# Performance work log

Hardware: AMD Instinct MI355X
Metric: run time of the kernel (lower is better)

Reference implementation:

```python
import jax, jax.numpy as jnp
import numpy as np

BOLTZMAN = 0.001987191
NATOM = 200000
L = 64  # filter_length


def setup_inputs() -> dict:
    key = jax.random.key(0)
    k1, k2, k3, k4, k5 = jax.random.split(key, 5)
    v = jax.random.normal(k1, (NATOM, 3), dtype=jnp.float32)
    mass = jnp.ones((NATOM, 3), dtype=jnp.float32)
    h = jax.random.uniform(k2, (1, 1, L), dtype=jnp.float32) * 0.002  # ~gamma_uniform scale
    v_list = jax.random.normal(k3, (NATOM * 3, 1, L), dtype=jnp.float32)
    w_list = jax.random.normal(k4, (NATOM * 3, 1, L), dtype=jnp.float32)
    w_new = jax.random.normal(k5, (NATOM, 3), dtype=jnp.float32)
    return {"v": v, "T": 300, "dt": 1, "mass": mass, "h": h,
            "v_list": v_list, "w_list": w_list, "w_new": w_new}


def reference(v, T, dt, mass, h, v_list, w_list, w_new):
    h1 = h[0, 0]  # [L]
    # construct_memory: conv1d(pad(h,(0,L-1)), h) == autocorrelation lags 0..L-1
    mk = jnp.correlate(h1, h1, mode="full")[L - 1:]  # [L]
    mk = mk * (mass[0, 0] * BOLTZMAN * T)
    # roll ring buffers left by 1 and write newest sample in last slot
    vl = jnp.concatenate([v_list[:, 0, 1:], v.reshape(-1, 1)], axis=1)   # [3N, L]
    wl = jnp.concatenate([w_list[:, 0, 1:], w_new.reshape(-1, 1)], axis=1)  # [3N, L]
    # conv1d(x, k.flip(2)) with len-L kernel -> single dot product per channel:
    # out = sum_t x[t] * k[L-1-t]
    friction = -(vl @ mk[::-1])          # [3N]
    random = wl @ h1[::-1]               # [3N]
    delta_v_langevin = (friction + random).reshape(v.shape)
    return delta_v_langevin
```

## Files before the change

### kernel.cpp

```cpp
#include <hip/hip_runtime.h>

#define BOLTZMAN 0.001987191f

__global__ void gle_setup(const float* __restrict__ h,
                          const float* __restrict__ mass,
                          const int* __restrict__ T,
                          float* __restrict__ coef) {
    __shared__ float sh[64];
    int t = threadIdx.x;
    if (t < 64) sh[t] = h[t];
    __syncthreads();
    if (t < 64) {
        float scale = mass[0] * BOLTZMAN * (float)T[0];
        int lag = (t == 0) ? 0 : (64 - t);
        float s = 0.0f;
        for (int k = 0; k + lag < 64; ++k) s += sh[k] * sh[k + lag];
        coef[t]      = -scale * s;
        coef[64 + t] = (t == 0) ? sh[0] : sh[64 - t];
    }
}

__global__ void __launch_bounds__(256) gle_main(
    const float* __restrict__ v, const float* __restrict__ w_new,
    const float* __restrict__ v_list, const float* __restrict__ w_list,
    const float* __restrict__ coef, float* __restrict__ out, int nrows)
{
    int row = blockIdx.x * 16 + (threadIdx.x >> 4);
    int c = threadIdx.x & 15;
    if (row >= nrows) return;

    const float4* A4 = (const float4*)coef;
    const float4* B4 = (const float4*)(coef + 64);
    float4 a = A4[c];
    float4 b = B4[c];

    float4 x = ((const float4*)(v_list + (size_t)row * 64))[c];
    float4 y = ((const float4*)(w_list + (size_t)row * 64))[c];
    if (c == 0) { x.x = v[row]; y.x = w_new[row]; }

    float s = a.x * x.x + a.y * x.y + a.z * x.z + a.w * x.w
            + b.x * y.x + b.y * y.y + b.z * y.z + b.w * y.w;

    s += __shfl_xor(s, 1);
    s += __shfl_xor(s, 2);
    s += __shfl_xor(s, 4);
    s += __shfl_xor(s, 8);

    if (c == 0) out[row] = s;
}

extern "C" void kernel_launch(void* const* d_in, const int* in_sizes, int n_in,
                              void* d_out, int out_size, void* d_ws, size_t ws_size,
                              hipStream_t stream) {
    const float* v      = (const float*)d_in[0];
    const int*   T      = (const int*)d_in[1];
    const float* mass   = (const float*)d_in[3];
    const float* h      = (const float*)d_in[4];
    const float* v_list = (const float*)d_in[5];
    const float* w_list = (const float*)d_in[6];
    const float* w_new  = (const float*)d_in[7];
    float* out  = (float*)d_out;
    float* coef = (float*)d_ws;

    int nrows = in_sizes[0];

    gle_setup<<<1, 64, 0, stream>>>(h, mass, T, coef);

    int blocks = (nrows + 15) / 16;
    gle_main<<<blocks, 256, 0, stream>>>(v, w_new, v_list, w_list, coef, out, nrows);
}
```

Before: 61.02 us.

## Fuse coefficient setup into main kernel, computing autocorrelation per block

Drops the separate single-block setup kernel. Each block of the main kernel now computes the autocorrelation memory kernel and reversed filter into shared memory before doing its row dot products. This removes one kernel launch and the global workspace round trip. In exchange, every block repeats the redundant O(L^2) prologue and waits on two barriers before issuing its streaming loads.

```diff
diff --git a/kernel.cpp b/kernel.cpp
--- a/kernel.cpp
+++ b/kernel.cpp
@@ -2,44 +2,46 @@
 
 #define BOLTZMAN 0.001987191f
 
-__global__ void gle_setup(const float* __restrict__ h,
-                          const float* __restrict__ mass,
-                          const int* __restrict__ T,
-                          float* __restrict__ coef) {
+__device__ __forceinline__ float rowdot(const float4 a, const float4 b,
+                                        const float4 x, const float4 y) {
+    return a.x * x.x + a.y * x.y + a.z * x.z + a.w * x.w
+         + b.x * y.x + b.y * y.y + b.z * y.z + b.w * y.w;
+}
+
+__global__ void __launch_bounds__(256) gle_fused(
+    const float* __restrict__ v, const float* __restrict__ w_new,
+    const float* __restrict__ v_list, const float* __restrict__ w_list,
+    const float* __restrict__ h, const float* __restrict__ mass,
+    const int* __restrict__ T, float* __restrict__ out, int nrows)
+{
     __shared__ float sh[64];
-    int t = threadIdx.x;
-    if (t < 64) sh[t] = h[t];
+    __shared__ float scoef[128];
+
+    const int tid = threadIdx.x;
+    if (tid < 64) sh[tid] = h[tid];
     __syncthreads();
-    if (t < 64) {
+    if (tid < 64) {
         float scale = mass[0] * BOLTZMAN * (float)T[0];
-        int lag = (t == 0) ? 0 : (64 - t);
+        int lag = (tid == 0) ? 0 : (64 - tid);
         float s = 0.0f;
         for (int k = 0; k + lag < 64; ++k) s += sh[k] * sh[k + lag];
-        coef[t]      = -scale * s;
-        coef[64 + t] = (t == 0) ? sh[0] : sh[64 - t];
+        scoef[tid]      = -scale * s;
+        scoef[64 + tid] = (tid == 0) ? sh[0] : sh[64 - tid];
     }
-}
+    __syncthreads();
 
-__global__ void __launch_bounds__(256) gle_main(
-    const float* __restrict__ v, const float* __restrict__ w_new,
-    const float* __restrict__ v_list, const float* __restrict__ w_list,
-    const float* __restrict__ coef, float* __restrict__ out, int nrows)
-{
-    int row = blockIdx.x * 16 + (threadIdx.x >> 4);
-    int c = threadIdx.x & 15;
+    const int row = blockIdx.x * 16 + (tid >> 4);
+    const int c = tid & 15;
     if (row >= nrows) return;
 
-    const float4* A4 = (const float4*)coef;
-    const float4* B4 = (const float4*)(coef + 64);
-    float4 a = A4[c];
-    float4 b = B4[c];
+    const float4 a = ((const float4*)scoef)[c];
+    const float4 b = ((const float4*)(scoef + 64))[c];
 
     float4 x = ((const float4*)(v_list + (size_t)row * 64))[c];
     float4 y = ((const float4*)(w_list + (size_t)row * 64))[c];
     if (c == 0) { x.x = v[row]; y.x = w_new[row]; }
 
-    float s = a.x * x.x + a.y * x.y + a.z * x.z + a.w * x.w
-            + b.x * y.x + b.y * y.y + b.z * y.z + b.w * y.w;
+    float s = rowdot(a, b, x, y);
 
     s += __shfl_xor(s, 1);
     s += __shfl_xor(s, 2);
@@ -60,12 +62,10 @@
     const float* w_list = (const float*)d_in[6];
     const float* w_new  = (const float*)d_in[7];
     float* out  = (float*)d_out;
-    float* coef = (float*)d_ws;
 
     int nrows = in_sizes[0];
 
-    gle_setup<<<1, 64, 0, stream>>>(h, mass, T, coef);
-
     int blocks = (nrows + 15) / 16;
-    gle_main<<<blocks, 256, 0, stream>>>(v, w_new, v_list, w_list, coef, out, nrows);
+    gle_fused<<<blocks, 256, 0, stream>>>(v, w_new, v_list, w_list,
+                                          h, mass, T, out, nrows);
 }
```

New measurement: 78.29 us. 1.28x slower.
